# Kernel optimization log

Hardware: AMD Instinct MI355X
Metric: run time of the kernel (lower is better)

The kernel has to match this reference:

```python
import jax, jax.numpy as jnp
import numpy as np

P_DROP = 0.6  # F.dropout default training=True in the original forward

def setup_inputs() -> dict:
    key = jax.random.key(0)
    k1, k2, k3, k4 = jax.random.split(key, 4)
    B, T, V, F, K, O = 32, 12, 1000, 64, 3, 64
    x = jax.random.normal(k1, (B, T, V, F), dtype=jnp.float32)
    Att = jax.random.uniform(k2, (V, V), dtype=jnp.float32)
    cheb = jax.random.normal(k3, (K, V, V), dtype=jnp.float32)   # Chebyshev polynomials T_k(L)
    Theta = jax.random.normal(k4, (K, F, O), dtype=jnp.float32)  # per-order feature transforms
    return {"x": x, "Att": Att, "cheb": cheb, "Theta": Theta}

def reference(x, Att, cheb, Theta):
    # x: [B,T,V,F]; Att: [V,V]; cheb: [K,V,V]; Theta: [K,F,O]
    B, T, V, F = x.shape
    K = cheb.shape[0]
    keep = 1.0 - P_DROP
    # Original draws a fresh dropout mask per (time_step, k); replicate with a fixed key.
    mask = jax.random.bernoulli(jax.random.key(42), keep, (T, K, V, V))
    TkA = cheb * Att                                   # [K,V,V] attention-weighted polynomial
    M = jnp.where(mask, TkA[None] / keep, 0.0)         # [T,K,V,V] inverted dropout
    # rhs = T_k_with_at @ graph_signal, batched over (b,t,k)
    rhs = jnp.einsum('tkuv,btvf->btkuf', M, x)         # [B,T,K,V,F]
    # sum_k rhs_k @ Theta_k  -> [B,T,V,O]; matches permute(0,3,1,2) of stacked outputs
    out = jnp.einsum('btkuf,kfo->btuo', rhs, Theta)
    return jax.nn.relu(out)
```

## Files before the change

### kernel.cpp

```cpp
#include <hip/hip_runtime.h>
#include <hip/hip_bf16.h>
#include <stdint.h>


typedef __attribute__((ext_vector_type(8))) short short8;
typedef __attribute__((ext_vector_type(4))) float f32x4;

__device__ __forceinline__ ushort f2bf(float f) {
  __hip_bfloat16 h = __float2bfloat16(f);
  return *reinterpret_cast<ushort*>(&h);
}

__device__ __forceinline__ void threefry2x32(uint32_t c0, uint32_t c1,
                                             uint32_t& o0, uint32_t& o1) {
  const uint32_t ks0 = 0u;
  const uint32_t ks1 = 42u;
  const uint32_t ks2 = ks0 ^ ks1 ^ 0x1BD11BDAu;
  uint32_t x0 = c0 + ks0;
  uint32_t x1 = c1 + ks1;
#define TFR(r) { x0 += x1; x1 = (x1 << (r)) | (x1 >> (32 - (r))); x1 ^= x0; }
  TFR(13) TFR(15) TFR(26) TFR(6)
  x0 += ks1; x1 += ks2 + 1u;
  TFR(17) TFR(29) TFR(16) TFR(24)
  x0 += ks2; x1 += ks0 + 2u;
  TFR(13) TFR(15) TFR(26) TFR(6)
  x0 += ks0; x1 += ks1 + 3u;
  TFR(17) TFR(29) TFR(16) TFR(24)
  x0 += ks1; x1 += ks2 + 4u;
  TFR(13) TFR(15) TFR(26) TFR(6)
  x0 += ks2; x1 += ks0 + 5u;
#undef TFR
  o0 = x0; o1 = x1;
}

__global__ void build_m(const float* __restrict__ Att,
                        const float* __restrict__ cheb,
                        ushort* __restrict__ Mws) {
  const uint32_t idx = blockIdx.x * 256u + threadIdx.x;
  const uint32_t vp = idx & 1023u;
  const uint32_t up = (idx >> 10) & 1023u;
  const uint32_t tk = idx >> 20;
  float val = 0.f;
  if ((vp < 1000u) & (up < 1000u)) {
    const uint32_t flat = (tk * 1000u + up) * 1000u + vp;
    uint32_t o0, o1;
    threefry2x32(0u, flat, o0, o1);
    const uint32_t bits = o0 ^ o1;
    const float u = __uint_as_float((bits >> 9) | 0x3f800000u) - 1.0f;
    if (u < 0.4f) {
      val = cheb[(tk % 3u) * 1000000u + up * 1000u + vp] *
            Att[up * 1000u + vp] * 2.5f;
    }
  }
  Mws[idx] = f2bf(val);
}

__global__ void transpose_x(const float* __restrict__ x,
                            ushort* __restrict__ xt) {
  __shared__ float lt[64][65];
  const int vc = blockIdx.x, t = blockIdx.y, b = blockIdx.z;
  const int tid = threadIdx.x;
  const int v0 = vc * 64;
#pragma unroll
  for (int i = 0; i < 4; ++i) {
    const int c = i * 256 + tid;
    const int vi = c >> 4, f4 = c & 15;
    float4 q = make_float4(0.f, 0.f, 0.f, 0.f);
    if (v0 + vi < 1000)
      q = *(const float4*)(x + ((((size_t)b * 12 + t) * 1000 + v0 + vi) << 6) + f4 * 4);
    lt[f4 * 4 + 0][vi] = q.x;
    lt[f4 * 4 + 1][vi] = q.y;
    lt[f4 * 4 + 2][vi] = q.z;
    lt[f4 * 4 + 3][vi] = q.w;
  }
  __syncthreads();
  const int f = tid >> 2, g = tid & 3;
  alignas(16) ushort tmp[16];
#pragma unroll
  for (int j = 0; j < 16; ++j) tmp[j] = f2bf(lt[f][g * 16 + j]);
  const size_t base = ((size_t)(t * 2048 + b * 64 + f)) << 10;
  *(uint4*)(xt + base + v0 + g * 16)     = *(const uint4*)&tmp[0];
  *(uint4*)(xt + base + v0 + g * 16 + 8) = *(const uint4*)&tmp[8];
}

#define LDT 72

__device__ __forceinline__ f32x4 mfma_bf16(short8 a, short8 b, f32x4 c) {
  asm volatile("v_mfma_f32_16x16x32_bf16 %0, %1, %2, %0"
               : "+v"(c) : "v"(a), "v"(b));
  return c;
}

__global__ __launch_bounds__(512, 3)
void cheb_main(const ushort* __restrict__ Mws, const ushort* __restrict__ xt,
               const float* __restrict__ Theta, float* __restrict__ out) {
  __shared__ __align__(16) ushort smem[23040];
  const int tid = threadIdx.x;
  const int lane = tid & 63;
  const int w = tid >> 6;
  const int wu = w >> 1, wn = w & 1;
  const int quad = lane >> 4, l15 = lane & 15;
  const int nt = blockIdx.x, ut = blockIdx.y, t = blockIdx.z;
  const int u0 = ut * 128, n0 = nt * 128;

  ushort* sA  = smem;
  ushort* sB  = smem + 8192;
  ushort* sP  = smem + w * (32 * LDT);
  ushort* sTh = smem + 8 * 32 * LDT;

  const int srow = lane >> 3;
  const int schunk = lane & 7;
  const int gchunk = schunk ^ srow;
  const int rsw = l15 & 7;

  f32x4 oacc[2][4];
#pragma unroll
  for (int i = 0; i < 2; ++i)
#pragma unroll
    for (int j = 0; j < 4; ++j) oacc[i][j] = f32x4{0.f, 0.f, 0.f, 0.f};

  for (int kk = 0; kk < 3; ++kk) {
    __syncthreads();
    for (int e = tid; e < 4096; e += 512) {
      const int f = e >> 6, o = e & 63;
      sTh[o * LDT + f] = f2bf(Theta[kk * 4096 + e]);
    }

    f32x4 pacc[2][4];
#pragma unroll
    for (int i = 0; i < 2; ++i)
#pragma unroll
      for (int j = 0; j < 4; ++j) pacc[i][j] = f32x4{0.f, 0.f, 0.f, 0.f};

    const size_t mbase = (size_t)(t * 3 + kk) << 20;
    const size_t xrow0 = (size_t)(t * 2048 + n0);

    for (int vc = 0; vc < 16; ++vc) {
      __syncthreads();
#pragma unroll
      for (int j = 0; j < 2; ++j) {
        const int rr = 8 * (w * 2 + j) + srow;
        const uint4 va = *(const uint4*)(Mws + mbase +
                          ((size_t)(u0 + rr) << 10) + vc * 64 + gchunk * 8);
        *(uint4*)&sA[(w * 2 + j) * 512 + lane * 8] = va;
        const uint4 vb = *(const uint4*)(xt +
                          ((xrow0 + rr) << 10) + vc * 64 + gchunk * 8);
        *(uint4*)&sB[(w * 2 + j) * 512 + lane * 8] = vb;
      }
      __syncthreads();
#pragma unroll
      for (int ks = 0; ks < 2; ++ks) {
        short8 av[2], bv[4];
#pragma unroll
        for (int mi = 0; mi < 2; ++mi) {
          const int row = wu * 32 + mi * 16 + l15;
          const int c = (ks * 4 + quad) ^ rsw;
          av[mi] = *(const short8*)&sA[row * 64 + c * 8];
        }
#pragma unroll
        for (int ni = 0; ni < 4; ++ni) {
          const int row = wn * 64 + ni * 16 + l15;
          const int c = (ks * 4 + quad) ^ rsw;
          bv[ni] = *(const short8*)&sB[row * 64 + c * 8];
        }
#pragma unroll
        for (int mi = 0; mi < 2; ++mi)
#pragma unroll
          for (int ni = 0; ni < 4; ++ni)
            pacc[mi][ni] = mfma_bf16(av[mi], bv[ni], pacc[mi][ni]);
      }
    }

    __syncthreads();
#pragma unroll
    for (int mi = 0; mi < 2; ++mi)
#pragma unroll
      for (int ni = 0; ni < 4; ++ni)
#pragma unroll
        for (int r = 0; r < 4; ++r)
          sP[(mi * 16 + quad * 4 + r) * LDT + ni * 16 + l15] = f2bf(pacc[mi][ni][r]);
    __syncthreads();
#pragma unroll
    for (int ks = 0; ks < 2; ++ks) {
      short8 a2[2], b2[4];
#pragma unroll
      for (int mi = 0; mi < 2; ++mi)
        a2[mi] = *(const short8*)&sP[(mi * 16 + l15) * LDT + ks * 32 + quad * 8];
#pragma unroll
      for (int ni = 0; ni < 4; ++ni)
        b2[ni] = *(const short8*)&sTh[(ni * 16 + l15) * LDT + ks * 32 + quad * 8];
#pragma unroll
      for (int mi = 0; mi < 2; ++mi)
#pragma unroll
        for (int ni = 0; ni < 4; ++ni)
          oacc[mi][ni] = mfma_bf16(a2[mi], b2[ni], oacc[mi][ni]);
    }
  }

#pragma unroll
  for (int mi = 0; mi < 2; ++mi) {
    const int u_base = u0 + wu * 32 + mi * 16 + quad * 4;
#pragma unroll
    for (int ni = 0; ni < 4; ++ni) {
      const int n = n0 + wn * 64 + ni * 16 + l15;
      const int b = n >> 6, oo = n & 63;
      float* op = out + (((size_t)b * 12 + t) * 1000) * 64 + oo;
#pragma unroll
      for (int r = 0; r < 4; ++r) {
        const int u = u_base + r;
        if (u < 1000) op[(size_t)u * 64] = fmaxf(oacc[mi][ni][r], 0.f);
      }
    }
  }
}

extern "C" void kernel_launch(void* const* d_in, const int* in_sizes, int n_in,
                              void* d_out, int out_size, void* d_ws, size_t ws_size,
                              hipStream_t stream) {
  const float* x     = (const float*)d_in[0];
  const float* Att   = (const float*)d_in[1];
  const float* cheb  = (const float*)d_in[2];
  const float* Theta = (const float*)d_in[3];
  float* out = (float*)d_out;

  ushort* Mws = (ushort*)d_ws;
  ushort* xtw = Mws + 37748736ull;

  build_m<<<147456, 256, 0, stream>>>(Att, cheb, Mws);
  transpose_x<<<dim3(16, 12, 32), 256, 0, stream>>>(x, xtw);
  cheb_main<<<dim3(16, 8, 12), 512, 0, stream>>>(Mws, xtw, Theta, out);
}
```

Baseline: 310.7 us.

## Fuse all three Chebyshev orders into one pass with register-prefetched tiles

The main kernel now loads the three M tiles for all Chebyshev orders plus one x tile per step, and keeps three sets of accumulators. This way each x tile is loaded once instead of three times. Global loads for the next chunk are issued into registers before the MFMAs of the current chunk and written to shared memory afterwards, and wave priority is raised during compute. The cost is more registers and more shared memory, so occupancy drops from three to two blocks per CU. The Theta projection then runs over the three orders once the loop ends.

Result: slower. 841.5 us (+170.9%).

```diff
diff --git a/kernel.cpp b/kernel.cpp
--- a/kernel.cpp
+++ b/kernel.cpp
@@ -91,10 +91,10 @@
   return c;
 }
 
-__global__ __launch_bounds__(512, 3)
+__global__ __launch_bounds__(512, 2)
 void cheb_main(const ushort* __restrict__ Mws, const ushort* __restrict__ xt,
                const float* __restrict__ Theta, float* __restrict__ out) {
-  __shared__ __align__(16) ushort smem[23040];
+  __shared__ __align__(16) ushort smem[32768];
   const int tid = threadIdx.x;
   const int lane = tid & 63;
   const int w = tid >> 6;
@@ -104,82 +104,110 @@
   const int u0 = ut * 128, n0 = nt * 128;
 
   ushort* sA  = smem;
-  ushort* sB  = smem + 8192;
+  ushort* sB  = smem + 24576;
   ushort* sP  = smem + w * (32 * LDT);
-  ushort* sTh = smem + 8 * 32 * LDT;
+  ushort* sTh = smem + 24576;
 
   const int srow = lane >> 3;
-  const int schunk = lane & 7;
-  const int gchunk = schunk ^ srow;
+  const int gchunk = (lane & 7) ^ srow;
   const int rsw = l15 & 7;
 
+  const size_t mbase = (size_t)(t * 3) << 20;
+  const size_t xrow0 = (size_t)(t * 2048 + n0);
+
+  uint4 pf[8];
+  auto issue = [&](int vc) {
+#pragma unroll
+    for (int q = 0; q < 8; ++q) {
+      const int r = q >> 1, j = q & 1;
+      const int rr = 8 * (w * 2 + j) + srow;
+      const ushort* src = (r < 3)
+          ? Mws + mbase + ((size_t)r << 20) + ((size_t)(u0 + rr) << 10) + vc * 64 + gchunk * 8
+          : xt + ((xrow0 + rr) << 10) + vc * 64 + gchunk * 8;
+      pf[q] = *(const uint4*)src;
+    }
+  };
+  auto commit = [&]() {
+#pragma unroll
+    for (int q = 0; q < 8; ++q) {
+      const int r = q >> 1, j = q & 1;
+      ushort* dst = (r < 3) ? sA + r * 8192 + (w * 2 + j) * 512 + lane * 8
+                            : sB + (w * 2 + j) * 512 + lane * 8;
+      *(uint4*)dst = pf[q];
+    }
+  };
+
+  f32x4 pacc[3][2][4];
+#pragma unroll
+  for (int k = 0; k < 3; ++k)
+#pragma unroll
+    for (int i = 0; i < 2; ++i)
+#pragma unroll
+      for (int j = 0; j < 4; ++j) pacc[k][i][j] = f32x4{0.f, 0.f, 0.f, 0.f};
+
+  issue(0);
+  commit();
+  asm volatile("s_waitcnt lgkmcnt(0)" ::: "memory");
+  __builtin_amdgcn_s_barrier();
+
+#pragma unroll 1
+  for (int vc = 0; vc < 16; ++vc) {
+    if (vc < 15) issue(vc + 1);
+    __builtin_amdgcn_s_setprio(1);
+#pragma unroll
+    for (int ks = 0; ks < 2; ++ks) {
+      short8 bv[4];
+#pragma unroll
+      for (int ni = 0; ni < 4; ++ni) {
+        const int row = wn * 64 + ni * 16 + l15;
+        bv[ni] = *(const short8*)&sB[row * 64 + (((ks * 4 + quad) ^ rsw) * 8)];
+      }
+#pragma unroll
+      for (int k = 0; k < 3; ++k) {
+        short8 av[2];
+#pragma unroll
+        for (int mi = 0; mi < 2; ++mi) {
+          const int row = wu * 32 + mi * 16 + l15;
+          av[mi] = *(const short8*)&sA[k * 8192 + row * 64 + (((ks * 4 + quad) ^ rsw) * 8)];
+        }
+#pragma unroll
+        for (int mi = 0; mi < 2; ++mi)
+#pragma unroll
+          for (int ni = 0; ni < 4; ++ni)
+            pacc[k][mi][ni] = mfma_bf16(av[mi], bv[ni], pacc[k][mi][ni]);
+      }
+    }
+    __builtin_amdgcn_s_setprio(0);
+    __builtin_amdgcn_s_barrier();
+    if (vc < 15) {
+      commit();
+      asm volatile("s_waitcnt lgkmcnt(0)" ::: "memory");
+      __builtin_amdgcn_sched_barrier(0);
+      __builtin_amdgcn_s_barrier();
+    }
+  }
+
   f32x4 oacc[2][4];
 #pragma unroll
   for (int i = 0; i < 2; ++i)
 #pragma unroll
     for (int j = 0; j < 4; ++j) oacc[i][j] = f32x4{0.f, 0.f, 0.f, 0.f};
 
-  for (int kk = 0; kk < 3; ++kk) {
-    __syncthreads();
+#pragma unroll 1
+  for (int k = 0; k < 3; ++k) {
+#pragma unroll
+    for (int mi = 0; mi < 2; ++mi)
+#pragma unroll
+      for (int ni = 0; ni < 4; ++ni)
+#pragma unroll
+        for (int r = 0; r < 4; ++r)
+          sP[(mi * 16 + quad * 4 + r) * LDT + ni * 16 + l15] = f2bf(pacc[k][mi][ni][r]);
     for (int e = tid; e < 4096; e += 512) {
       const int f = e >> 6, o = e & 63;
-      sTh[o * LDT + f] = f2bf(Theta[kk * 4096 + e]);
-    }
-
-    f32x4 pacc[2][4];
-#pragma unroll
-    for (int i = 0; i < 2; ++i)
-#pragma unroll
-      for (int j = 0; j < 4; ++j) pacc[i][j] = f32x4{0.f, 0.f, 0.f, 0.f};
-
-    const size_t mbase = (size_t)(t * 3 + kk) << 20;
-    const size_t xrow0 = (size_t)(t * 2048 + n0);
-
-    for (int vc = 0; vc < 16; ++vc) {
-      __syncthreads();
-#pragma unroll
-      for (int j = 0; j < 2; ++j) {
-        const int rr = 8 * (w * 2 + j) + srow;
-        const uint4 va = *(const uint4*)(Mws + mbase +
-                          ((size_t)(u0 + rr) << 10) + vc * 64 + gchunk * 8);
-        *(uint4*)&sA[(w * 2 + j) * 512 + lane * 8] = va;
-        const uint4 vb = *(const uint4*)(xt +
-                          ((xrow0 + rr) << 10) + vc * 64 + gchunk * 8);
-        *(uint4*)&sB[(w * 2 + j) * 512 + lane * 8] = vb;
-      }
-      __syncthreads();
-#pragma unroll
-      for (int ks = 0; ks < 2; ++ks) {
-        short8 av[2], bv[4];
-#pragma unroll
-        for (int mi = 0; mi < 2; ++mi) {
-          const int row = wu * 32 + mi * 16 + l15;
-          const int c = (ks * 4 + quad) ^ rsw;
-          av[mi] = *(const short8*)&sA[row * 64 + c * 8];
-        }
-#pragma unroll
-        for (int ni = 0; ni < 4; ++ni) {
-          const int row = wn * 64 + ni * 16 + l15;
-          const int c = (ks * 4 + quad) ^ rsw;
-          bv[ni] = *(const short8*)&sB[row * 64 + c * 8];
-        }
-#pragma unroll
-        for (int mi = 0; mi < 2; ++mi)
-#pragma unroll
-          for (int ni = 0; ni < 4; ++ni)
-            pacc[mi][ni] = mfma_bf16(av[mi], bv[ni], pacc[mi][ni]);
-      }
-    }
-
-    __syncthreads();
-#pragma unroll
-    for (int mi = 0; mi < 2; ++mi)
-#pragma unroll
-      for (int ni = 0; ni < 4; ++ni)
-#pragma unroll
-        for (int r = 0; r < 4; ++r)
-          sP[(mi * 16 + quad * 4 + r) * LDT + ni * 16 + l15] = f2bf(pacc[mi][ni][r]);
-    __syncthreads();
+      sTh[o * LDT + f] = f2bf(Theta[k * 4096 + e]);
+    }
+    asm volatile("s_waitcnt lgkmcnt(0)" ::: "memory");
+    __builtin_amdgcn_s_barrier();
 #pragma unroll
     for (int ks = 0; ks < 2; ++ks) {
       short8 a2[2], b2[4];
@@ -195,6 +223,7 @@
         for (int ni = 0; ni < 4; ++ni)
           oacc[mi][ni] = mfma_bf16(a2[mi], b2[ni], oacc[mi][ni]);
     }
+    __builtin_amdgcn_s_barrier();
   }
 
 #pragma unroll
```
